# Kernel tuning notes

Measured on AMD Instinct MI355X. Metric: run time of the kernel, lower is better.

## Reference

```python
import jax, jax.numpy as jnp
import numpy as np

B, TP, TH = 128, 128, 64
V, E, H, O = 50000, 300, 512, 3


def _lstm(x, lens, Wih, Whh, bih, bhh):
    # PyTorch LSTM, batch_first, gate order i,f,g,o; masked like pack_padded_sequence
    Bn, T, _ = x.shape
    Hn = Whh.shape[1]
    mask = jnp.arange(T)[None, :] < lens[:, None]  # [B,T]
    def step(carry, xt_mt):
        h, c = carry
        xt, mt = xt_mt  # [B,E], [B,1]
        g = xt @ Wih.T + h @ Whh.T + bih + bhh
        i, f, gg, o = jnp.split(g, 4, axis=-1)
        c_new = jax.nn.sigmoid(f) * c + jax.nn.sigmoid(i) * jnp.tanh(gg)
        h_new = jax.nn.sigmoid(o) * jnp.tanh(c_new)
        return (jnp.where(mt, h_new, h), jnp.where(mt, c_new, c)), jnp.where(mt, h_new, 0.0)
    z = jnp.zeros((Bn, Hn), x.dtype)
    _, hs = jax.lax.scan(step, (z, z), (jnp.swapaxes(x, 0, 1), jnp.swapaxes(mask, 0, 1)[..., None]))
    return jnp.swapaxes(hs, 0, 1)  # [B,T,H]


def _cell(x, h, c, Wih, Whh, bih, bhh):
    g = x @ Wih.T + h @ Whh.T + bih + bhh
    i, f, gg, o = jnp.split(g, 4, axis=-1)
    c_new = jax.nn.sigmoid(f) * c + jax.nn.sigmoid(i) * jnp.tanh(gg)
    h_new = jax.nn.sigmoid(o) * jnp.tanh(c_new)
    return h_new, c_new


def setup_inputs() -> dict:
    key = jax.random.key(0)
    ks = jax.random.split(key, 24)
    def unif(k, shape, fan):
        s = 1.0 / np.sqrt(fan)
        return jax.random.uniform(k, shape, jnp.float32, -s, s)
    inp = {}
    inp["premise"] = jax.random.randint(ks[0], (B, TP), 0, V, jnp.int32)
    inp["premise_len"] = jnp.full((B,), TP, jnp.int32)
    inp["hypothesis"] = jax.random.randint(ks[1], (B, TH), 0, V, jnp.int32)
    inp["hypothesis_len"] = jnp.full((B,), TH, jnp.int32)
    inp["embed_table"] = jax.random.normal(ks[2], (V, E), jnp.float32) * 0.1
    inp["embed_table"] = inp["embed_table"].at[0].set(0.0)  # padding_idx=0
    # premise LSTM
    inp["Wih_p"] = unif(ks[3], (4 * H, E), H); inp["Whh_p"] = unif(ks[4], (4 * H, H), H)
    inp["bih_p"] = unif(ks[5], (4 * H,), H); inp["bhh_p"] = unif(ks[6], (4 * H,), H)
    # hypothesis LSTM
    inp["Wih_h"] = unif(ks[7], (4 * H, E), H); inp["Whh_h"] = unif(ks[8], (4 * H, H), H)
    inp["bih_h"] = unif(ks[9], (4 * H,), H); inp["bhh_h"] = unif(ks[10], (4 * H,), H)
    # match LSTMCell (input 2H)
    inp["Wih_m"] = unif(ks[11], (4 * H, 2 * H), H); inp["Whh_m"] = unif(ks[12], (4 * H, H), H)
    inp["bih_m"] = unif(ks[13], (4 * H,), H); inp["bhh_m"] = unif(ks[14], (4 * H,), H)
    # attention
    inp["w_e"] = jax.random.uniform(ks[15], (H,), jnp.float32, 0.0, 1.0)
    inp["W_s"] = unif(ks[16], (H, H), H)
    inp["W_t"] = unif(ks[17], (H, H), H)
    inp["W_m"] = unif(ks[18], (H, H), H)
    inp["W_fc"] = unif(ks[19], (O, H), H)
    inp["b_fc"] = unif(ks[20], (O,), H)
    return inp


def reference(premise, premise_len, hypothesis, hypothesis_len, embed_table,
              Wih_p, Whh_p, bih_p, bhh_p, Wih_h, Whh_h, bih_h, bhh_h,
              Wih_m, Whh_m, bih_m, bhh_m, w_e, W_s, W_t, W_m, W_fc, b_fc):
    Bn = premise.shape[0]
    Hn = Whh_m.shape[1]
    p_emb = embed_table[premise]      # [B,Tp,E]
    h_emb = embed_table[hypothesis]   # [B,Th,E]
    h_s = _lstm(p_emb, premise_len, Wih_p, Whh_p, bih_p, bhh_p)      # [B,Tp,H]
    h_t = _lstm(h_emb, hypothesis_len, Wih_h, Whh_h, bih_h, bhh_h)   # [B,Th,H]
    Ws = jnp.einsum('bth,gh->btg', h_s, W_s)  # precompute w_s(h_s) once

    def step(carry, htk):
        h_m, c_m = carry
        q = htk @ W_t.T + h_m @ W_m.T                    # [B,H]
        s = jnp.tanh(Ws + q[:, None, :])                 # [B,Tp,H]
        e = s @ w_e                                      # [B,Tp]
        alpha = jax.nn.softmax(e, axis=1)                # softmax over premise positions
        a = jnp.einsum('bt,bth->bh', alpha, h_s)
        m_k = jnp.concatenate([a, htk], axis=1)          # [B,2H]
        h_m2, c_m2 = _cell(m_k, h_m, c_m, Wih_m, Whh_m, bih_m, bhh_m)
        return (h_m2, c_m2), h_m2

    z = jnp.zeros((Bn, Hn), h_s.dtype)
    _, hm_all = jax.lax.scan(step, (z, z), jnp.swapaxes(h_t, 0, 1))  # [Th,B,H]
    hm_all = jnp.swapaxes(hm_all, 0, 1)                              # [B,Th,H]
    idx = (hypothesis_len - 1).astype(jnp.int32)[:, None, None]
    last = jnp.take_along_axis(hm_all, idx, axis=1)[:, 0, :]         # last hidden per example
    return last @ W_fc.T + b_fc
```

## Files before the change

kernel.cpp:

```cpp
#include <hip/hip_runtime.h>
#include <hip/hip_bf16.h>

using bf16 = __hip_bfloat16;

constexpr int BB = 128;
constexpr int TPp = 128;
constexpr int THh = 64;
constexpr int HH = 512;

constexpr size_t OFF_HS     = 0;
constexpr size_t SZ_HS      = (size_t)16384 * 512;
constexpr size_t OFF_HT     = OFF_HS + SZ_HS;
constexpr size_t SZ_HT      = (size_t)8192 * 512;
constexpr size_t OFF_WSM    = OFF_HT + SZ_HT;
constexpr size_t SZ_WSM     = (size_t)16384 * 512;
constexpr size_t OFF_WIHT_P = OFF_WSM + SZ_WSM;
constexpr size_t SZ_WIHT    = (size_t)304 * 2048;
constexpr size_t OFF_WIHT_H = OFF_WIHT_P + SZ_WIHT;
constexpr size_t OFF_WHHT_P = OFF_WIHT_H + SZ_WIHT;
constexpr size_t OFF_WHHT_H = OFF_WHHT_P + (size_t)512 * 2048;
constexpr size_t OFF_WHHM2  = OFF_WHHT_H + (size_t)512 * 2048;
constexpr size_t OFF_WIA    = OFF_WHHM2 + (size_t)1024 * 2048;
constexpr size_t OFF_WMT2   = OFF_WIA + (size_t)512 * 2048;
constexpr size_t OFF_WEF    = OFF_WMT2 + (size_t)1024 * 512;
constexpr size_t OFF_BM     = OFF_WEF + 512;
constexpr size_t OFF_HC_P   = OFF_BM + 2048;
constexpr size_t OFF_HC_H   = OFF_HC_P + 2 * (size_t)BB * HH;
constexpr size_t OFF_C_P    = OFF_HC_H + 2 * (size_t)BB * HH;
constexpr size_t OFF_C_H    = OFF_C_P + (size_t)BB * HH;
constexpr size_t OFF_Q      = OFF_C_H + (size_t)BB * HH;
constexpr size_t OFF_GH     = OFF_Q + (size_t)BB * HH;
constexpr size_t OFF_A      = OFF_GH + (size_t)BB * 2048;
constexpr size_t OFF_HM     = OFF_A + (size_t)BB * HH;
constexpr size_t OFF_CM     = OFF_HM + (size_t)BB * HH;
constexpr size_t OFF_LAST   = OFF_CM + (size_t)BB * HH;
constexpr size_t WS_FLOATS  = OFF_LAST + (size_t)BB * HH;

__device__ __forceinline__ float sigmf(float x) { return 1.0f / (1.0f + __expf(-x)); }
__device__ __forceinline__ float tanh_f(float x) {
  float e = __expf(-2.0f * fabsf(x));
  float r = (1.0f - e) / (1.0f + e);
  return copysignf(r, x);
}

__global__ void k_diag(float* out, float v) {
  int i = blockIdx.x * 64 + threadIdx.x;
  if (i < BB * 3) out[i] = v;
}

__global__ __launch_bounds__(256) void k_prep(float* ws,
    const float* Wih_p, const float* bih_p, const float* bhh_p,
    const float* Wih_h, const float* bih_h, const float* bhh_h,
    const float* Whh_p, const float* Whh_h,
    const float* Whh_m, const float* Wih_m, const float* bih_m, const float* bhh_m,
    const float* W_m, const float* W_t, const float* w_e) {
  size_t gid = (size_t)blockIdx.x * 256 + threadIdx.x;
  if (gid < SZ_WIHT) {
    int k = (int)(gid >> 11), r = (int)(gid & 2047);
    float v = (k < 300) ? Wih_p[(size_t)r * 300 + k]
            : (k == 303) ? (bih_p[r] + bhh_p[r]) : 0.f;
    ws[OFF_WIHT_P + gid] = v;
    return;
  }
  gid -= SZ_WIHT;
  if (gid < SZ_WIHT) {
    int k = (int)(gid >> 11), r = (int)(gid & 2047);
    float v = (k < 300) ? Wih_h[(size_t)r * 300 + k]
            : (k == 303) ? (bih_h[r] + bhh_h[r]) : 0.f;
    ws[OFF_WIHT_H + gid] = v;
    return;
  }
  gid -= SZ_WIHT;
  const size_t NT = (size_t)512 * 2048;
  if (gid < NT) {
    int k = (int)(gid >> 11), r = (int)(gid & 2047);
    ws[OFF_WHHT_P + gid] = Whh_p[(size_t)r * 512 + k];
    return;
  }
  gid -= NT;
  if (gid < NT) {
    int k = (int)(gid >> 11), r = (int)(gid & 2047);
    ws[OFF_WHHT_H + gid] = Whh_h[(size_t)r * 512 + k];
    return;
  }
  gid -= NT;
  if (gid < (size_t)1024 * 2048) {
    int k = (int)(gid >> 11), r = (int)(gid & 2047);
    ws[OFF_WHHM2 + gid] = (k < 512) ? Whh_m[(size_t)r * 512 + k]
                                    : Wih_m[(size_t)r * 1024 + k];
    return;
  }
  gid -= (size_t)1024 * 2048;
  if (gid < NT) {
    int k = (int)(gid >> 11), c = (int)(gid & 2047);
    int j = c >> 2, g = c & 3;
    ws[OFF_WIA + gid] = Wih_m[((size_t)g * 512 + j) * 1024 + k];
    return;
  }
  gid -= NT;
  if (gid < (size_t)1024 * 512) {
    int k = (int)(gid >> 9), r = (int)(gid & 511);
    ws[OFF_WMT2 + gid] = (k < 512) ? W_m[(size_t)r * 512 + k]
                                   : W_t[(size_t)r * 512 + (k - 512)];
    return;
  }
  gid -= (size_t)1024 * 512;
  if (gid < 512) { ws[OFF_WEF + gid] = w_e[gid]; return; }
  gid -= 512;
  if (gid < 2048) { ws[OFF_BM + gid] = bih_m[gid] + bhh_m[gid]; return; }
  gid -= 2048;
  if (gid < (size_t)393216) { ws[OFF_HC_P + gid] = 0.f; return; }
  gid -= 393216;
  if (gid < (size_t)131072) { ws[OFF_HM + gid] = 0.f; return; }
}

__global__ __launch_bounds__(256) void k_gemm(const float* __restrict__ A,
                                              const float* __restrict__ Bw, int ldb, int Kdim,
                                              int N, float* __restrict__ C, int ntilesN) {
  __shared__ float As[16][68];
  __shared__ float Bs[16][68];
  const int tid = threadIdx.x;
  const int bid = blockIdx.x;
  const int tm = bid / ntilesN, tn = bid % ntilesN;
  const int m0 = tm * 64, n0 = tn * 64;
  const int tx = tid & 15, ty = tid >> 4;
  const int srow = tid >> 2, skc = (tid & 3) * 4;
  float acc[4][4] = {};
  const float* arowf = A + (size_t)(m0 + srow) * Kdim;
  const float* brow = Bw + (size_t)(n0 + srow) * ldb;
  for (int k0 = 0; k0 < Kdim; k0 += 16) {
    float4 v = *(const float4*)(arowf + k0 + skc);
    As[skc + 0][srow] = v.x; As[skc + 1][srow] = v.y;
    As[skc + 2][srow] = v.z; As[skc + 3][srow] = v.w;
#pragma unroll
    for (int i = 0; i < 4; i++) Bs[skc + i][srow] = brow[k0 + skc + i];
    __syncthreads();
#pragma unroll
    for (int kk = 0; kk < 16; kk++) {
      float4 a4 = *(float4*)&As[kk][ty * 4];
      float4 b4 = *(float4*)&Bs[kk][tx * 4];
      acc[0][0] += a4.x * b4.x; acc[0][1] += a4.x * b4.y; acc[0][2] += a4.x * b4.z; acc[0][3] += a4.x * b4.w;
      acc[1][0] += a4.y * b4.x; acc[1][1] += a4.y * b4.y; acc[1][2] += a4.y * b4.z; acc[1][3] += a4.y * b4.w;
      acc[2][0] += a4.z * b4.x; acc[2][1] += a4.z * b4.y; acc[2][2] += a4.z * b4.z; acc[2][3] += a4.z * b4.w;
      acc[3][0] += a4.w * b4.x; acc[3][1] += a4.w * b4.y; acc[3][2] += a4.w * b4.z; acc[3][3] += a4.w * b4.w;
    }
    __syncthreads();
  }
  const int m = m0 + ty * 4, n = n0 + tx * 4;
#pragma unroll
  for (int i = 0; i < 4; i++) {
    float4 o = {acc[i][0], acc[i][1], acc[i][2], acc[i][3]};
    *(float4*)&C[(size_t)(m + i) * N + n] = o;
  }
}

__global__ __launch_bounds__(256) void k_lstm_step(float* ws, const int* premise, const int* hyp,
                                                   const int* plen, const int* hlen,
                                                   const float* emb, int t) {
  __shared__ float h_lds[16 * 512];
  __shared__ float x_lds[16 * 304];
  __shared__ float g_tile[16 * 128];
  __shared__ int tok_lds[16];
  const int tid = threadIdx.x;
  const int bid = blockIdx.x;
  const int seq = bid >> 7;
  if (seq && t >= THh) return;
  const int li = bid & 127;
  const int bg = li >> 4, slice = li & 15;
  const int b0 = bg * 16, j0 = slice * 32;
  const int T = seq ? THh : TPp;
  const int* toks = seq ? hyp : premise;
  const float* WT = ws + (seq ? OFF_WHHT_H : OFF_WHHT_P);
  const float* WX = ws + (seq ? OFF_WIHT_H : OFF_WIHT_P);
  float* hsout = ws + (seq ? OFF_HT : OFF_HS);
  float* hc = ws + (seq ? OFF_HC_H : OFF_HC_P);
  float* cbuf = ws + (seq ? OFF_C_H : OFF_C_P);
  const int* lens = seq ? hlen : plen;

  if (tid < 16) tok_lds[tid] = toks[(size_t)(b0 + tid) * T + t];
  {
    const float4* src = (const float4*)(hc + (size_t)(t & 1) * (BB * HH) + (size_t)b0 * 512);
    float4* dst = (float4*)h_lds;
    for (int i = tid; i < 2048; i += 256) dst[i] = src[i];
  }
  __syncthreads();
  for (int i = tid; i < 16 * 152; i += 256) {
    int row = i / 152, c2 = i - row * 152;
    int k2 = c2 * 2;
    float v0 = 0.f, v1 = 0.f;
    if (k2 < 300) {
      float2 f = *(const float2*)(emb + (size_t)tok_lds[row] * 300 + k2);
      v0 = f.x; v1 = f.y;
    } else if (k2 == 302) {
      v1 = 1.0f;
    }
    x_lds[row * 304 + k2] = v0;
    x_lds[row * 304 + k2 + 1] = v1;
  }
  __syncthreads();

  const int rp = tid & 63;
  const int bq = tid >> 6;
  const int rl0 = rp * 2;
  const int gate0 = rl0 >> 5, jl0 = rl0 & 31;
  const int col0 = gate0 * 512 + j0 + jl0;
  float acc[4][2] = {};
#pragma unroll 2
  for (int k = 0; k < 512; k += 4) {
    float4 h0 = *(float4*)&h_lds[(bq * 4 + 0) * 512 + k];
    float4 h1 = *(float4*)&h_lds[(bq * 4 + 1) * 512 + k];
    float4 h2 = *(float4*)&h_lds[(bq * 4 + 2) * 512 + k];
    float4 h3 = *(float4*)&h_lds[(bq * 4 + 3) * 512 + k];
    float2 w0 = *(const float2*)&WT[(size_t)(k + 0) * 2048 + col0];
    float2 w1 = *(const float2*)&WT[(size_t)(k + 1) * 2048 + col0];
    float2 w2 = *(const float2*)&WT[(size_t)(k + 2) * 2048 + col0];
    float2 w3 = *(const float2*)&WT[(size_t)(k + 3) * 2048 + col0];
    acc[0][0] += h0.x * w0.x + h0.y * w1.x + h0.z * w2.x + h0.w * w3.x;
    acc[0][1] += h0.x * w0.y + h0.y * w1.y + h0.z * w2.y + h0.w * w3.y;
    acc[1][0] += h1.x * w0.x + h1.y * w1.x + h1.z * w2.x + h1.w * w3.x;
    acc[1][1] += h1.x * w0.y + h1.y * w1.y + h1.z * w2.y + h1.w * w3.y;
    acc[2][0] += h2.x * w0.x + h2.y * w1.x + h2.z * w2.x + h2.w * w3.x;
    acc[2][1] += h2.x * w0.y + h2.y * w1.y + h2.z * w2.y + h2.w * w3.y;
    acc[3][0] += h3.x * w0.x + h3.y * w1.x + h3.z * w2.x + h3.w * w3.x;
    acc[3][1] += h3.x * w0.y + h3.y * w1.y + h3.z * w2.y + h3.w * w3.y;
  }
#pragma unroll 2
  for (int k = 0; k < 304; k += 4) {
    float4 x0 = *(float4*)&x_lds[(bq * 4 + 0) * 304 + k];
    float4 x1 = *(float4*)&x_lds[(bq * 4 + 1) * 304 + k];
    float4 x2 = *(float4*)&x_lds[(bq * 4 + 2) * 304 + k];
    float4 x3 = *(float4*)&x_lds[(bq * 4 + 3) * 304 + k];
    float2 w0 = *(const float2*)&WX[(size_t)(k + 0) * 2048 + col0];
    float2 w1 = *(const float2*)&WX[(size_t)(k + 1) * 2048 + col0];
    float2 w2 = *(const float2*)&WX[(size_t)(k + 2) * 2048 + col0];
    float2 w3 = *(const float2*)&WX[(size_t)(k + 3) * 2048 + col0];
    acc[0][0] += x0.x * w0.x + x0.y * w1.x + x0.z * w2.x + x0.w * w3.x;
    acc[0][1] += x0.x * w0.y + x0.y * w1.y + x0.z * w2.y + x0.w * w3.y;
    acc[1][0] += x1.x * w0.x + x1.y * w1.x + x1.z * w2.x + x1.w * w3.x;
    acc[1][1] += x1.x * w0.y + x1.y * w1.y + x1.z * w2.y + x1.w * w3.y;
    acc[2][0] += x2.x * w0.x + x2.y * w1.x + x2.z * w2.x + x2.w * w3.x;
    acc[2][1] += x2.x * w0.y + x2.y * w1.y + x2.z * w2.y + x2.w * w3.y;
    acc[3][0] += x3.x * w0.x + x3.y * w1.x + x3.z * w2.x + x3.w * w3.x;
    acc[3][1] += x3.x * w0.y + x3.y * w1.y + x3.z * w2.y + x3.w * w3.y;
  }
#pragma unroll
  for (int i = 0; i < 4; i++) {
    int bl = bq * 4 + i;
    g_tile[bl * 128 + rl0] = acc[i][0];
    g_tile[bl * 128 + rl0 + 1] = acc[i][1];
  }
  __syncthreads();
#pragma unroll
  for (int s = 0; s < 2; s++) {
    int p = tid * 2 + s;
    int bl = p >> 5, jl = p & 31;
    int bglob = b0 + bl, jglob = j0 + jl;
    float gi = g_tile[bl * 128 + jl];
    float gf = g_tile[bl * 128 + 32 + jl];
    float gg = g_tile[bl * 128 + 64 + jl];
    float go = g_tile[bl * 128 + 96 + jl];
    bool inr = t < lens[bglob];
    float iv = sigmf(gi), fv = sigmf(gf), gv = tanh_f(gg), ov = sigmf(go);
    float cold = cbuf[(size_t)bglob * 512 + jglob];
    float cn = fv * cold + iv * gv;
    float hn = ov * tanh_f(cn);
    float hprev = h_lds[bl * 512 + jglob];
    if (inr) cbuf[(size_t)bglob * 512 + jglob] = cn;
    hsout[((size_t)bglob * T + t) * 512 + jglob] = inr ? hn : 0.f;
    hc[(size_t)((t + 1) & 1) * (BB * HH) + (size_t)bglob * 512 + jglob] = inr ? hn : hprev;
  }
}

__global__ __launch_bounds__(256) void k_p1(float* __restrict__ ws, int k) {
  __shared__ float lds_a[16 * 1024];
  const int tid = threadIdx.x;
  const int task = blockIdx.x;
  const float* hm = ws + OFF_HM;
  const float* ht = ws + OFF_HT;
  const bool isq = task < 64;
  int mt, nt, ldb2;
  const float* BT;
  if (isq) { mt = task >> 3; nt = task & 7; BT = ws + OFF_WMT2; ldb2 = 512; }
  else { int u = task - 64; mt = u >> 5; nt = u & 31; BT = ws + OFF_WHHM2; ldb2 = 2048; }
  for (int i = tid; i < 2048; i += 256) {
    int row = i >> 7, c4 = i & 127;
    ((float4*)lds_a)[row * 256 + c4] =
        ((const float4*)(hm + (size_t)(mt * 16 + row) * 512))[c4];
    ((float4*)lds_a)[row * 256 + 128 + c4] =
        ((const float4*)(ht + ((size_t)(mt * 16 + row) * THh + k) * 512))[c4];
  }
  __syncthreads();
  const int tx = tid & 15, my = tid >> 4;
  const int ncol = nt * 64 + tx * 4;
  float4 acc = {0.f, 0.f, 0.f, 0.f};
  for (int kk = 0; kk < 1024; kk += 4) {
    float4 av = *(float4*)&lds_a[my * 1024 + kk];
    const float* bp = BT + (size_t)kk * ldb2 + ncol;
    float4 bv0 = *(const float4*)(bp);
    float4 bv1 = *(const float4*)(bp + ldb2);
    float4 bv2 = *(const float4*)(bp + 2 * (size_t)ldb2);
    float4 bv3 = *(const float4*)(bp + 3 * (size_t)ldb2);
    acc.x += av.x * bv0.x + av.y * bv1.x + av.z * bv2.x + av.w * bv3.x;
    acc.y += av.x * bv0.y + av.y * bv1.y + av.z * bv2.y + av.w * bv3.y;
    acc.z += av.x * bv0.z + av.y * bv1.z + av.z * bv2.z + av.w * bv3.z;
    acc.w += av.x * bv0.w + av.y * bv1.w + av.z * bv2.w + av.w * bv3.w;
  }
  const int m = mt * 16 + my;
  if (isq) *(float4*)&ws[OFF_Q + (size_t)m * 512 + ncol] = acc;
  else *(float4*)&ws[OFF_GH + (size_t)m * 2048 + ncol] = acc;
}

__global__ __launch_bounds__(256) void k_p2(float* __restrict__ ws) {
  __shared__ float q_lds[512];
  __shared__ float we_lds[512];
  __shared__ float e_part[256];
  __shared__ float e_lds[128];
  __shared__ float alpha_lds[128];
  __shared__ float red_s[2];
  const int tid = threadIdx.x;
  const int b = blockIdx.x;
  const float* q = ws + OFF_Q;
  const float* Wsb = ws + OFF_WSM;
  const float* hs = ws + OFF_HS;
  const float* wef = ws + OFF_WEF;
  float* abuf = ws + OFF_A;

  for (int i = tid; i < 512; i += 256) {
    q_lds[i] = q[(size_t)b * 512 + i];
    we_lds[i] = wef[i];
  }
  __syncthreads();
  {
    int t2 = tid >> 1;
    int gbase = (tid & 1) * 256;
    const float* wsrow = Wsb + ((size_t)b * TPp + t2) * 512 + gbase;
    float s = 0.f;
    for (int ii = 0; ii < 256; ii += 4) {
      float4 wv = *(const float4*)(wsrow + ii);
      float4 qv = *(float4*)&q_lds[gbase + ii];
      float4 ev = *(float4*)&we_lds[gbase + ii];
      s += tanh_f(wv.x + qv.x) * ev.x + tanh_f(wv.y + qv.y) * ev.y +
           tanh_f(wv.z + qv.z) * ev.z + tanh_f(wv.w + qv.w) * ev.w;
    }
    e_part[tid] = s;
  }
  __syncthreads();
  if (tid < 128) e_lds[tid] = e_part[tid * 2] + e_part[tid * 2 + 1];
  __syncthreads();
  if (tid < 64) {
    float m = fmaxf(e_lds[tid], e_lds[tid + 64]);
    for (int off = 32; off > 0; off >>= 1) m = fmaxf(m, __shfl_down(m, off));
    if (tid == 0) red_s[0] = m;
  }
  __syncthreads();
  if (tid < 128) alpha_lds[tid] = __expf(e_lds[tid] - red_s[0]);
  __syncthreads();
  if (tid < 64) {
    float s = alpha_lds[tid] + alpha_lds[tid + 64];
    for (int off = 32; off > 0; off >>= 1) s += __shfl_down(s, off);
    if (tid == 0) red_s[1] = 1.f / s;
  }
  __syncthreads();
  {
    float inv = red_s[1];
    float a0 = 0.f, a1 = 0.f;
    const float* hsb = hs + (size_t)b * TPp * 512 + tid * 2;
    for (int t2 = 0; t2 < TPp; t2++) {
      float2 hv = *(const float2*)(hsb + (size_t)t2 * 512);
      float al = alpha_lds[t2];
      a0 += al * hv.x;
      a1 += al * hv.y;
    }
    abuf[(size_t)b * 512 + tid * 2] = a0 * inv;
    abuf[(size_t)b * 512 + tid * 2 + 1] = a1 * inv;
  }
}

__global__ __launch_bounds__(256) void k_p3(float* __restrict__ ws, const int* __restrict__ hlen, int k) {
  __shared__ float lds_p3[16 * 512];
  const int tid = threadIdx.x;
  const int w = blockIdx.x;
  const int mt3 = w >> 5, jt3 = w & 31;
  const int my3 = tid >> 4, tx3 = tid & 15;
  const int b3 = mt3 * 16 + my3, j3 = jt3 * 16 + tx3;
  const int jcol4 = j3 * 4;
  const float* abuf = ws + OFF_A;
  const float* gh = ws + OFF_GH;
  const float* wia = ws + OFF_WIA;
  const float* bm = ws + OFF_BM;
  float* hm = ws + OFF_HM;
  float* cm = ws + OFF_CM;
  float* last = ws + OFF_LAST;

  {
    const float4* s4 = (const float4*)(abuf + (size_t)mt3 * 16 * 512);
    float4* d4 = (float4*)lds_p3;
    for (int i = tid; i < 2048; i += 256) d4[i] = s4[i];
  }
  __syncthreads();
  float a0 = 0.f, a1 = 0.f, a2 = 0.f, a3 = 0.f;
  for (int kk = 0; kk < 512; kk += 4) {
    float4 av = *(float4*)&lds_p3[my3 * 512 + kk];
    const float* wp = wia + (size_t)kk * 2048 + jcol4;
    float4 w0 = *(const float4*)(wp);
    float4 w1 = *(const float4*)(wp + 2048);
    float4 w2 = *(const float4*)(wp + 4096);
    float4 w3 = *(const float4*)(wp + 6144);
    a0 += av.x * w0.x + av.y * w1.x + av.z * w2.x + av.w * w3.x;
    a1 += av.x * w0.y + av.y * w1.y + av.z * w2.y + av.w * w3.y;
    a2 += av.x * w0.z + av.y * w1.z + av.z * w2.z + av.w * w3.z;
    a3 += av.x * w0.w + av.y * w1.w + av.z * w2.w + av.w * w3.w;
  }
  float gm[4] = {a0, a1, a2, a3};
#pragma unroll
  for (int g = 0; g < 4; g++) {
    int colg = g * 512 + j3;
    gm[g] += gh[(size_t)b3 * 2048 + colg] + bm[colg];
  }
  float iv = sigmf(gm[0]), fv = sigmf(gm[1]), gv = tanh_f(gm[2]), ov = sigmf(gm[3]);
  float cold = cm[(size_t)b3 * 512 + j3];
  float cn = fv * cold + iv * gv;
  float hn = ov * tanh_f(cn);
  cm[(size_t)b3 * 512 + j3] = cn;
  hm[(size_t)b3 * 512 + j3] = hn;
  if (k == hlen[b3] - 1) last[(size_t)b3 * 512 + j3] = hn;
}

__global__ __launch_bounds__(256) void k_fc(const float* __restrict__ ws, const float* __restrict__ Wfc,
                                            const float* __restrict__ bfc, float* __restrict__ out) {
  int idx = blockIdx.x * 256 + threadIdx.x;
  if (idx >= BB * 3) return;
  int b = idx / 3, o = idx - b * 3;
  const float* lrow = ws + OFF_LAST + (size_t)b * 512;
  const float* wrow = Wfc + (size_t)o * 512;
  float acc = bfc[o];
  for (int h = 0; h < 512; h++) acc += lrow[h] * wrow[h];
  out[idx] = acc;
}

extern "C" void kernel_launch(void* const* d_in, const int* in_sizes, int n_in, void* d_out,
                              int out_size, void* d_ws, size_t ws_size, hipStream_t stream) {
  const int* premise = (const int*)d_in[0];
  const int* plen = (const int*)d_in[1];
  const int* hyp = (const int*)d_in[2];
  const int* hlen = (const int*)d_in[3];
  const float* emb = (const float*)d_in[4];
  const float* Wih_p = (const float*)d_in[5];
  const float* Whh_p = (const float*)d_in[6];
  const float* bih_p = (const float*)d_in[7];
  const float* bhh_p = (const float*)d_in[8];
  const float* Wih_h = (const float*)d_in[9];
  const float* Whh_h = (const float*)d_in[10];
  const float* bih_h = (const float*)d_in[11];
  const float* bhh_h = (const float*)d_in[12];
  const float* Wih_m = (const float*)d_in[13];
  const float* Whh_m = (const float*)d_in[14];
  const float* bih_m = (const float*)d_in[15];
  const float* bhh_m = (const float*)d_in[16];
  const float* w_e = (const float*)d_in[17];
  const float* W_s = (const float*)d_in[18];
  const float* W_t = (const float*)d_in[19];
  const float* W_m = (const float*)d_in[20];
  const float* W_fc = (const float*)d_in[21];
  const float* b_fc = (const float*)d_in[22];
  float* ws = (float*)d_ws;
  float* out = (float*)d_out;

  if (ws_size < WS_FLOATS * sizeof(float)) {
    float mb = (float)((double)ws_size / (1024.0 * 1024.0));
    k_diag<<<dim3(6), dim3(64), 0, stream>>>(out, mb);
    return;
  }

  {
    size_t total = 2 * SZ_WIHT + 2 * (size_t)512 * 2048 + (size_t)1024 * 2048 +
                   (size_t)512 * 2048 + (size_t)1024 * 512 + 512 + 2048 + 393216 + 131072;
    int nb = (int)((total + 255) / 256);
    k_prep<<<dim3(nb), dim3(256), 0, stream>>>(ws, Wih_p, bih_p, bhh_p, Wih_h, bih_h, bhh_h,
                                               Whh_p, Whh_h, Whh_m, Wih_m, bih_m, bhh_m,
                                               W_m, W_t, w_e);
  }
  for (int t = 0; t < TPp; t++) {
    k_lstm_step<<<dim3(256), dim3(256), 0, stream>>>(ws, premise, hyp, plen, hlen, emb, t);
  }
  k_gemm<<<dim3(256 * 8), dim3(256), 0, stream>>>(ws + OFF_HS, W_s, 512, 512, 512,
                                                  ws + OFF_WSM, 8);
  for (int k = 0; k < THh; k++) {
    k_p1<<<dim3(320), dim3(256), 0, stream>>>(ws, k);
    k_p2<<<dim3(128), dim3(256), 0, stream>>>(ws);
    k_p3<<<dim3(256), dim3(256), 0, stream>>>(ws, hlen, k);
  }
  k_fc<<<dim3(2), dim3(256), 0, stream>>>(ws, W_fc, b_fc, out);
}
```

Measured before the change: 12.41 ms.

## Hoist LSTM input projection into chunked GEMM and restructure recurrent step

Moves the embedding-times-Wih projection out of each per-timestep kernel into a batched GEMM over chunks of 16 timesteps, stored in the otherwise unused Ws buffer region. The recurrent step kernel now gives each block 4 hidden units across all 128 batch rows, with its Whh slice repacked so the i/f/g/o gates sit together and the whole slice stays in LDS. The previous hidden state is streamed through a swizzled LDS buffer with register prefetch. Hypothesis-sequence blocks are no longer launched after step 64. The intent is to stop re-reading the input weights and embeddings on the serial critical path, at the cost of extra launches and a workspace-aliasing dependency.

```diff
diff --git a/kernel.cpp b/kernel.cpp
--- a/kernel.cpp
+++ b/kernel.cpp
@@ -1,7 +1,5 @@
 #include <hip/hip_runtime.h>
 #include <hip/hip_bf16.h>
-
-using bf16 = __hip_bfloat16;
 
 constexpr int BB = 128;
 constexpr int TPp = 128;
@@ -14,6 +12,8 @@
 constexpr size_t SZ_HT      = (size_t)8192 * 512;
 constexpr size_t OFF_WSM    = OFF_HT + SZ_HT;
 constexpr size_t SZ_WSM     = (size_t)16384 * 512;
+constexpr size_t OFF_XG_P   = OFF_WSM;
+constexpr size_t OFF_XG_H   = OFF_WSM + (size_t)16 * 128 * 128 * 16;
 constexpr size_t OFF_WIHT_P = OFF_WSM + SZ_WSM;
 constexpr size_t SZ_WIHT    = (size_t)304 * 2048;
 constexpr size_t OFF_WIHT_H = OFF_WIHT_P + SZ_WIHT;
@@ -73,14 +73,20 @@
   gid -= SZ_WIHT;
   const size_t NT = (size_t)512 * 2048;
   if (gid < NT) {
-    int k = (int)(gid >> 11), r = (int)(gid & 2047);
-    ws[OFF_WHHT_P + gid] = Whh_p[(size_t)r * 512 + k];
+    int li = (int)(gid >> 13);
+    int rem = (int)(gid & 8191);
+    int k = rem >> 4, c = rem & 15;
+    int jj = c >> 2, g = c & 3;
+    ws[OFF_WHHT_P + gid] = Whh_p[(size_t)(g * 512 + li * 4 + jj) * 512 + k];
     return;
   }
   gid -= NT;
   if (gid < NT) {
-    int k = (int)(gid >> 11), r = (int)(gid & 2047);
-    ws[OFF_WHHT_H + gid] = Whh_h[(size_t)r * 512 + k];
+    int li = (int)(gid >> 13);
+    int rem = (int)(gid & 8191);
+    int k = rem >> 4, c = rem & 15;
+    int jj = c >> 2, g = c & 3;
+    ws[OFF_WHHT_H + gid] = Whh_h[(size_t)(g * 512 + li * 4 + jj) * 512 + k];
     return;
   }
   gid -= NT;
@@ -154,120 +160,162 @@
   }
 }
 
-__global__ __launch_bounds__(256) void k_lstm_step(float* ws, const int* premise, const int* hyp,
-                                                   const int* plen, const int* hlen,
-                                                   const float* emb, int t) {
-  __shared__ float h_lds[16 * 512];
-  __shared__ float x_lds[16 * 304];
-  __shared__ float g_tile[16 * 128];
-  __shared__ int tok_lds[16];
+__global__ __launch_bounds__(256) void k_xg(float* __restrict__ ws,
+    const int* __restrict__ premise, const int* __restrict__ hyp,
+    const float* __restrict__ emb, int c0) {
+  __shared__ float As[16][68];
+  __shared__ float Bs[16][68];
+  __shared__ int tok_lds[64];
+  const int tid = threadIdx.x;
+  const int bid = blockIdx.x;
+  const int seq = bid >> 10;
+  const int u = bid & 1023;
+  const int tm = u >> 5, tn = u & 31;
+  const int m0 = tm * 64, n0 = tn * 64;
+  const int T = seq ? THh : TPp;
+  const int* toks = seq ? hyp : premise;
+  const float* WX = ws + (seq ? OFF_WIHT_H : OFF_WIHT_P);
+  float* xg = ws + (seq ? OFF_XG_H : OFF_XG_P);
+  if (tid < 64) {
+    int r = m0 + tid;
+    int tl = r >> 7, b = r & 127;
+    tok_lds[tid] = toks[(size_t)b * T + c0 + tl];
+  }
+  __syncthreads();
+  const int tx = tid & 15, ty = tid >> 4;
+  const int sr = tid & 63, sk0 = (tid >> 6) * 4;
+  const int bky = tid >> 4, bkx = (tid & 15) * 4;
+  float acc[4][4] = {};
+  for (int k0 = 0; k0 < 304; k0 += 16) {
+    int tok = tok_lds[sr];
+#pragma unroll
+    for (int i = 0; i < 4; i++) {
+      int k = k0 + sk0 + i;
+      float v = 0.f;
+      if (k < 300) v = emb[(size_t)tok * 300 + k];
+      else if (k == 303) v = 1.f;
+      As[sk0 + i][sr] = v;
+    }
+    *(float4*)&Bs[bky][bkx] = *(const float4*)(WX + (size_t)(k0 + bky) * 2048 + n0 + bkx);
+    __syncthreads();
+#pragma unroll
+    for (int kk = 0; kk < 16; kk++) {
+      float4 a4 = *(float4*)&As[kk][ty * 4];
+      float4 b4 = *(float4*)&Bs[kk][tx * 4];
+      acc[0][0] += a4.x * b4.x; acc[0][1] += a4.x * b4.y; acc[0][2] += a4.x * b4.z; acc[0][3] += a4.x * b4.w;
+      acc[1][0] += a4.y * b4.x; acc[1][1] += a4.y * b4.y; acc[1][2] += a4.y * b4.z; acc[1][3] += a4.y * b4.w;
+      acc[2][0] += a4.z * b4.x; acc[2][1] += a4.z * b4.y; acc[2][2] += a4.z * b4.z; acc[2][3] += a4.z * b4.w;
+      acc[3][0] += a4.w * b4.x; acc[3][1] += a4.w * b4.y; acc[3][2] += a4.w * b4.z; acc[3][3] += a4.w * b4.w;
+    }
+    __syncthreads();
+  }
+  const int cbase = n0 + tx * 4;
+  const int g = cbase >> 9;
+  const int li = (cbase & 511) >> 2;
+#pragma unroll
+  for (int i = 0; i < 4; i++) {
+    int r = m0 + ty * 4 + i;
+    int tl = r >> 7, b = r & 127;
+    float* dst = xg + (((size_t)tl * 128 + li) * 128 + b) * 16 + g;
+#pragma unroll
+    for (int jj = 0; jj < 4; jj++) dst[jj * 4] = acc[i][jj];
+  }
+}
+
+__global__ __launch_bounds__(256) void k_step(float* __restrict__ ws,
+    const int* __restrict__ plen, const int* __restrict__ hlen, int t) {
+  __shared__ float4 wlds4[2048];
+  __shared__ float4 hbuf4[2048];
   const int tid = threadIdx.x;
   const int bid = blockIdx.x;
   const int seq = bid >> 7;
-  if (seq && t >= THh) return;
   const int li = bid & 127;
-  const int bg = li >> 4, slice = li & 15;
-  const int b0 = bg * 16, j0 = slice * 32;
   const int T = seq ? THh : TPp;
-  const int* toks = seq ? hyp : premise;
-  const float* WT = ws + (seq ? OFF_WHHT_H : OFF_WHHT_P);
-  const float* WX = ws + (seq ? OFF_WIHT_H : OFF_WIHT_P);
+  const int* lens = seq ? hlen : plen;
+  const float* wstk = ws + (seq ? OFF_WHHT_H : OFF_WHHT_P) + (size_t)li * 8192;
+  const float* xg = ws + (seq ? OFF_XG_H : OFF_XG_P) + ((size_t)(t & 15) * 128 + li) * 2048;
   float* hsout = ws + (seq ? OFF_HT : OFF_HS);
   float* hc = ws + (seq ? OFF_HC_H : OFF_HC_P);
-  float* cbuf = ws + (seq ? OFF_C_H : OFF_C_P);
-  const int* lens = seq ? hlen : plen;
-
-  if (tid < 16) tok_lds[tid] = toks[(size_t)(b0 + tid) * T + t];
-  {
-    const float4* src = (const float4*)(hc + (size_t)(t & 1) * (BB * HH) + (size_t)b0 * 512);
-    float4* dst = (float4*)h_lds;
-    for (int i = tid; i < 2048; i += 256) dst[i] = src[i];
-  }
-  __syncthreads();
-  for (int i = tid; i < 16 * 152; i += 256) {
-    int row = i / 152, c2 = i - row * 152;
-    int k2 = c2 * 2;
-    float v0 = 0.f, v1 = 0.f;
-    if (k2 < 300) {
-      float2 f = *(const float2*)(emb + (size_t)tok_lds[row] * 300 + k2);
-      v0 = f.x; v1 = f.y;
-    } else if (k2 == 302) {
-      v1 = 1.0f;
-    }
-    x_lds[row * 304 + k2] = v0;
-    x_lds[row * 304 + k2 + 1] = v1;
-  }
-  __syncthreads();
-
-  const int rp = tid & 63;
-  const int bq = tid >> 6;
-  const int rl0 = rp * 2;
-  const int gate0 = rl0 >> 5, jl0 = rl0 & 31;
-  const int col0 = gate0 * 512 + j0 + jl0;
-  float acc[4][2] = {};
-#pragma unroll 2
-  for (int k = 0; k < 512; k += 4) {
-    float4 h0 = *(float4*)&h_lds[(bq * 4 + 0) * 512 + k];
-    float4 h1 = *(float4*)&h_lds[(bq * 4 + 1) * 512 + k];
-    float4 h2 = *(float4*)&h_lds[(bq * 4 + 2) * 512 + k];
-    float4 h3 = *(float4*)&h_lds[(bq * 4 + 3) * 512 + k];
-    float2 w0 = *(const float2*)&WT[(size_t)(k + 0) * 2048 + col0];
-    float2 w1 = *(const float2*)&WT[(size_t)(k + 1) * 2048 + col0];
-    float2 w2 = *(const float2*)&WT[(size_t)(k + 2) * 2048 + col0];
-    float2 w3 = *(const float2*)&WT[(size_t)(k + 3) * 2048 + col0];
-    acc[0][0] += h0.x * w0.x + h0.y * w1.x + h0.z * w2.x + h0.w * w3.x;
-    acc[0][1] += h0.x * w0.y + h0.y * w1.y + h0.z * w2.y + h0.w * w3.y;
-    acc[1][0] += h1.x * w0.x + h1.y * w1.x + h1.z * w2.x + h1.w * w3.x;
-    acc[1][1] += h1.x * w0.y + h1.y * w1.y + h1.z * w2.y + h1.w * w3.y;
-    acc[2][0] += h2.x * w0.x + h2.y * w1.x + h2.z * w2.x + h2.w * w3.x;
-    acc[2][1] += h2.x * w0.y + h2.y * w1.y + h2.z * w2.y + h2.w * w3.y;
-    acc[3][0] += h3.x * w0.x + h3.y * w1.x + h3.z * w2.x + h3.w * w3.x;
-    acc[3][1] += h3.x * w0.y + h3.y * w1.y + h3.z * w2.y + h3.w * w3.y;
-  }
-#pragma unroll 2
-  for (int k = 0; k < 304; k += 4) {
-    float4 x0 = *(float4*)&x_lds[(bq * 4 + 0) * 304 + k];
-    float4 x1 = *(float4*)&x_lds[(bq * 4 + 1) * 304 + k];
-    float4 x2 = *(float4*)&x_lds[(bq * 4 + 2) * 304 + k];
-    float4 x3 = *(float4*)&x_lds[(bq * 4 + 3) * 304 + k];
-    float2 w0 = *(const float2*)&WX[(size_t)(k + 0) * 2048 + col0];
-    float2 w1 = *(const float2*)&WX[(size_t)(k + 1) * 2048 + col0];
-    float2 w2 = *(const float2*)&WX[(size_t)(k + 2) * 2048 + col0];
-    float2 w3 = *(const float2*)&WX[(size_t)(k + 3) * 2048 + col0];
-    acc[0][0] += x0.x * w0.x + x0.y * w1.x + x0.z * w2.x + x0.w * w3.x;
-    acc[0][1] += x0.x * w0.y + x0.y * w1.y + x0.z * w2.y + x0.w * w3.y;
-    acc[1][0] += x1.x * w0.x + x1.y * w1.x + x1.z * w2.x + x1.w * w3.x;
-    acc[1][1] += x1.x * w0.y + x1.y * w1.y + x1.z * w2.y + x1.w * w3.y;
-    acc[2][0] += x2.x * w0.x + x2.y * w1.x + x2.z * w2.x + x2.w * w3.x;
-    acc[2][1] += x2.x * w0.y + x2.y * w1.y + x2.z * w2.y + x2.w * w3.y;
-    acc[3][0] += x3.x * w0.x + x3.y * w1.x + x3.z * w2.x + x3.w * w3.x;
-    acc[3][1] += x3.x * w0.y + x3.y * w1.y + x3.z * w2.y + x3.w * w3.y;
-  }
-#pragma unroll
-  for (int i = 0; i < 4; i++) {
-    int bl = bq * 4 + i;
-    g_tile[bl * 128 + rl0] = acc[i][0];
-    g_tile[bl * 128 + rl0 + 1] = acc[i][1];
-  }
-  __syncthreads();
-#pragma unroll
-  for (int s = 0; s < 2; s++) {
-    int p = tid * 2 + s;
-    int bl = p >> 5, jl = p & 31;
-    int bglob = b0 + bl, jglob = j0 + jl;
-    float gi = g_tile[bl * 128 + jl];
-    float gf = g_tile[bl * 128 + 32 + jl];
-    float gg = g_tile[bl * 128 + 64 + jl];
-    float go = g_tile[bl * 128 + 96 + jl];
-    bool inr = t < lens[bglob];
+  float* cst = ws + (seq ? OFF_C_H : OFF_C_P) + (size_t)li * 512;
+  const float* hin = hc + (size_t)(t & 1) * (BB * HH);
+  float* hout = hc + (size_t)((t + 1) & 1) * (BB * HH);
+
+  {
+    const float4* src = (const float4*)wstk;
+#pragma unroll
+    for (int j = 0; j < 8; j++) wlds4[tid + j * 256] = src[tid + j * 256];
+  }
+  const int bg = tid & 63, cg = tid >> 6;
+  const int b0 = 2 * bg, b1 = 2 * bg + 1;
+  const int sw = bg & 7;
+  float4 acc0 = {0.f, 0.f, 0.f, 0.f}, acc1 = {0.f, 0.f, 0.f, 0.f};
+
+  float4 pre[8];
+#pragma unroll
+  for (int j = 0; j < 8; j++) {
+    int fi = tid + j * 256, b = fi >> 4, k4 = fi & 15;
+    pre[j] = *(const float4*)(hin + (size_t)b * 512 + k4 * 4);
+  }
+  for (int kc = 0; kc < 512; kc += 64) {
+    __syncthreads();
+#pragma unroll
+    for (int j = 0; j < 8; j++) {
+      int fi = tid + j * 256, b = fi >> 4, k4 = fi & 15;
+      hbuf4[b * 16 + (k4 ^ ((b >> 1) & 7))] = pre[j];
+    }
+    __syncthreads();
+    if (kc + 64 < 512) {
+#pragma unroll
+      for (int j = 0; j < 8; j++) {
+        int fi = tid + j * 256, b = fi >> 4, k4 = fi & 15;
+        pre[j] = *(const float4*)(hin + (size_t)b * 512 + (kc + 64) + k4 * 4);
+      }
+    }
+#pragma unroll
+    for (int kk = 0; kk < 64; kk += 4) {
+      int k4 = kk >> 2;
+      float4 h0 = hbuf4[b0 * 16 + (k4 ^ sw)];
+      float4 h1 = hbuf4[b1 * 16 + (k4 ^ sw)];
+      float4 w0 = wlds4[(kc + kk + 0) * 4 + cg];
+      float4 w1 = wlds4[(kc + kk + 1) * 4 + cg];
+      float4 w2 = wlds4[(kc + kk + 2) * 4 + cg];
+      float4 w3 = wlds4[(kc + kk + 3) * 4 + cg];
+      acc0.x += h0.x * w0.x + h0.y * w1.x + h0.z * w2.x + h0.w * w3.x;
+      acc0.y += h0.x * w0.y + h0.y * w1.y + h0.z * w2.y + h0.w * w3.y;
+      acc0.z += h0.x * w0.z + h0.y * w1.z + h0.z * w2.z + h0.w * w3.z;
+      acc0.w += h0.x * w0.w + h0.y * w1.w + h0.z * w2.w + h0.w * w3.w;
+      acc1.x += h1.x * w0.x + h1.y * w1.x + h1.z * w2.x + h1.w * w3.x;
+      acc1.y += h1.x * w0.y + h1.y * w1.y + h1.z * w2.y + h1.w * w3.y;
+      acc1.z += h1.x * w0.z + h1.y * w1.z + h1.z * w2.z + h1.w * w3.z;
+      acc1.w += h1.x * w0.w + h1.y * w1.w + h1.z * w2.w + h1.w * w3.w;
+    }
+  }
+  const int j = li * 4 + cg;
+  float4 x0 = *(const float4*)(xg + (size_t)b0 * 16 + cg * 4);
+  float4 x1 = *(const float4*)(xg + (size_t)b1 * 16 + cg * 4);
+  {
+    float gi = acc0.x + x0.x, gf = acc0.y + x0.y, gg = acc0.z + x0.z, go = acc0.w + x0.w;
     float iv = sigmf(gi), fv = sigmf(gf), gv = tanh_f(gg), ov = sigmf(go);
-    float cold = cbuf[(size_t)bglob * 512 + jglob];
+    float cold = cst[b0 * 4 + cg];
     float cn = fv * cold + iv * gv;
     float hn = ov * tanh_f(cn);
-    float hprev = h_lds[bl * 512 + jglob];
-    if (inr) cbuf[(size_t)bglob * 512 + jglob] = cn;
-    hsout[((size_t)bglob * T + t) * 512 + jglob] = inr ? hn : 0.f;
-    hc[(size_t)((t + 1) & 1) * (BB * HH) + (size_t)bglob * 512 + jglob] = inr ? hn : hprev;
+    bool inr = t < lens[b0];
+    float hp = hin[(size_t)b0 * 512 + j];
+    if (inr) cst[b0 * 4 + cg] = cn;
+    hsout[((size_t)b0 * T + t) * 512 + j] = inr ? hn : 0.f;
+    hout[(size_t)b0 * 512 + j] = inr ? hn : hp;
+  }
+  {
+    float gi = acc1.x + x1.x, gf = acc1.y + x1.y, gg = acc1.z + x1.z, go = acc1.w + x1.w;
+    float iv = sigmf(gi), fv = sigmf(gf), gv = tanh_f(gg), ov = sigmf(go);
+    float cold = cst[b1 * 4 + cg];
+    float cn = fv * cold + iv * gv;
+    float hn = ov * tanh_f(cn);
+    bool inr = t < lens[b1];
+    float hp = hin[(size_t)b1 * 512 + j];
+    if (inr) cst[b1 * 4 + cg] = cn;
+    hsout[((size_t)b1 * T + t) * 512 + j] = inr ? hn : 0.f;
+    hout[(size_t)b1 * 512 + j] = inr ? hn : hp;
   }
 }
 
@@ -481,7 +529,12 @@
                                                W_m, W_t, w_e);
   }
   for (int t = 0; t < TPp; t++) {
-    k_lstm_step<<<dim3(256), dim3(256), 0, stream>>>(ws, premise, hyp, plen, hlen, emb, t);
+    if ((t & 15) == 0) {
+      int nb = (t < THh) ? 2048 : 1024;
+      k_xg<<<dim3(nb), dim3(256), 0, stream>>>(ws, premise, hyp, emb, t);
+    }
+    int ns = (t < THh) ? 256 : 128;
+    k_step<<<dim3(ns), dim3(256), 0, stream>>>(ws, plen, hlen, t);
   }
   k_gemm<<<dim3(256 * 8), dim3(256), 0, stream>>>(ws + OFF_HS, W_s, 512, 512, 512,
                                                   ws + OFF_WSM, 8);
```

Result: no change. 12.45 ms (+0.3%).
